# Kernel optimization log

Hardware: AMD Instinct MI355X
Metric: run time of the kernel (lower is better)

The kernel has to match this reference:

```python
import jax, jax.numpy as jnp
import numpy as np

N_NODES, N_EDGES, N_GRAPHS, D = 32768, 49152, 1024, 64


def setup_inputs() -> dict:
    key = jax.random.key(0)
    ks = jax.random.split(key, 24)
    p = lambda k, shape, s=0.1: jax.random.normal(k, shape, dtype=jnp.float32) * s
    return dict(
        x=jax.random.normal(ks[0], (N_NODES, 14), dtype=jnp.float32),
        edge_index=jax.random.randint(ks[1], (2, N_EDGES), 0, N_NODES),
        edge_attr=jax.random.uniform(ks[2], (N_EDGES, 4), dtype=jnp.float32),
        batch=jnp.sort(jax.random.randint(ks[3], (N_NODES,), 0, N_GRAPHS)),
        lin0_W=p(ks[4], (D, 14)), lin0_b=p(ks[5], (D,)),
        e1_W=p(ks[6], (128, 4)), e1_b=p(ks[7], (128,)),
        e2_W=p(ks[8], (D * D, 128), 0.02), e2_b=p(ks[9], (D * D,), 0.02),
        root_W=p(ks[10], (D, D)), conv_b=p(ks[11], (D,)),
        gru_Wih=p(ks[12], (3 * D, D)), gru_Whh=p(ks[13], (3 * D, D)),
        gru_bih=p(ks[14], (3 * D,)), gru_bhh=p(ks[15], (3 * D,)),
        lstm_Wih=p(ks[16], (4 * D, 2 * D)), lstm_Whh=p(ks[17], (4 * D, D)),
        lstm_bih=p(ks[18], (4 * D,)), lstm_bhh=p(ks[19], (4 * D,)),
        fc1_W=p(ks[20], (128, 2 * D)), fc1_b=p(ks[21], (128,)),
        fc2_W=p(ks[22], (1, 128)), fc2_b=p(ks[23], (1,)),
    )


def reference(x, edge_index, edge_attr, batch,
              lin0_W, lin0_b, e1_W, e1_b, e2_W, e2_b, root_W, conv_b,
              gru_Wih, gru_Whh, gru_bih, gru_bhh,
              lstm_Wih, lstm_Whh, lstm_bih, lstm_bhh,
              fc1_W, fc1_b, fc2_W, fc2_b):
    N, B = x.shape[0], N_GRAPHS
    src, dst = edge_index[0], edge_index[1]

    out = jax.nn.relu(x @ lin0_W.T + lin0_b)            # [N, D]
    h = out                                             # GRU hidden (num_layers=1)

    # Edge-conditioned weights: edge_attr is constant across the 3 iterations,
    # so compute the edge MLP once (identical math to re-running it).
    W = jax.nn.relu(edge_attr @ e1_W.T + e1_b) @ e2_W.T + e2_b
    W = W.reshape(-1, D, D)                             # [E, D, D]
    cnt = jnp.maximum(
        jax.ops.segment_sum(jnp.ones((src.shape[0],), x.dtype), dst, num_segments=N), 1.0)

    for _ in range(3):
        # NNConv (aggr='mean'): gather -> per-edge matmul -> scatter-mean -> root + bias
        msg = jnp.einsum('ei,eio->eo', out[src], W)     # [E, D]
        agg = jax.ops.segment_sum(msg, dst, num_segments=N) / cnt[:, None]
        m = jax.nn.relu(agg + out @ root_W + conv_b)
        # GRU cell (seq_len=1)
        gi = m @ gru_Wih.T + gru_bih
        gh = h @ gru_Whh.T + gru_bhh
        ir, iz, inn = jnp.split(gi, 3, -1)
        hr, hz, hn = jnp.split(gh, 3, -1)
        r = jax.nn.sigmoid(ir + hr)
        z = jax.nn.sigmoid(iz + hz)
        n = jnp.tanh(inn + r * hn)
        h = (1.0 - z) * n + z * h
        out = h

    # Set2Set pooling, 3 processing steps, LSTM(2D -> D)
    q_star = jnp.zeros((B, 2 * D), x.dtype)
    hl = jnp.zeros((B, D), x.dtype)
    cl = jnp.zeros((B, D), x.dtype)
    for _ in range(3):
        g = q_star @ lstm_Wih.T + lstm_bih + hl @ lstm_Whh.T + lstm_bhh
        i_, f_, g_, o_ = jnp.split(g, 4, -1)
        cl = jax.nn.sigmoid(f_) * cl + jax.nn.sigmoid(i_) * jnp.tanh(g_)
        hl = jax.nn.sigmoid(o_) * jnp.tanh(cl)
        q = hl                                          # [B, D]
        e = jnp.sum(out * q[batch], -1)                 # [N]
        mx = jax.ops.segment_max(e, batch, num_segments=B)
        ex = jnp.exp(e - mx[batch])
        den = jax.ops.segment_sum(ex, batch, num_segments=B)
        a = ex / den[batch]                             # segment softmax
        r_read = jax.ops.segment_sum(a[:, None] * out, batch, num_segments=B)
        q_star = jnp.concatenate([q, r_read], -1)       # [B, 2D]

    hid = jax.nn.relu(q_star @ fc1_W.T + fc1_b)
    return hid @ fc2_W.T + fc2_b                        # [B, 1]
```

## Files before the change

kernel.cpp:

```cpp
#include <hip/hip_runtime.h>
#include <math.h>

#define NN_ 32768
#define NE_ 49152
#define NG_ 1024

typedef short bh8 __attribute__((ext_vector_type(8)));
typedef float f32x4 __attribute__((ext_vector_type(4)));

__device__ __forceinline__ unsigned short f2bfu(float f) {
    union { float f; unsigned int i; } x; x.f = f;
    unsigned int u = x.i;
    u += 0x7FFFu + ((u >> 16) & 1u);
    return (unsigned short)(u >> 16);
}
__device__ __forceinline__ float sigm(float x) { return 1.f / (1.f + expf(-x)); }

__global__ void MPNN_78632261256134_kernel() {}

__global__ void k_init(int* deg, float* qstar, float* agg) {
    int i = blockIdx.x * 256 + threadIdx.x;
    if (i < NN_) deg[i] = 0;
    int j = i - NN_;
    if (j >= 0 && j < NG_ * 256) qstar[j] = 0.f;
    int k = i - NN_ - NG_ * 256;
    if (k >= 0 && k < NN_ * 64) agg[k] = 0.f;
}

__global__ void k_lin0(const float* x, const float* W, const float* b, float* node) {
    int g = blockIdx.x * 256 + threadIdx.x;
    int n = g >> 6, d = g & 63;
    const float* xr = x + n * 14;
    const float* wr = W + d * 14;
    float acc = b[d];
    for (int i = 0; i < 14; i++) acc += xr[i] * wr[i];
    node[g] = fmaxf(acc, 0.f);
}

__global__ void k_cnt(const int* dst, int* deg) {
    int e = blockIdx.x * 256 + threadIdx.x;
    if (e < NE_) atomicAdd(&deg[dst[e]], 1);
}

__global__ __launch_bounds__(256) void k_scanA(const int* __restrict__ deg,
                                               int* __restrict__ offs,
                                               int* __restrict__ bsum) {
    __shared__ int wtot[4];
    int tid = threadIdx.x, bid = blockIdx.x;
    int i = bid * 256 + tid;
    int v = deg[i];
    int sc = v;
    for (int o = 1; o < 64; o <<= 1) { int u = __shfl_up(sc, o); if ((tid & 63) >= o) sc += u; }
    if ((tid & 63) == 63) wtot[tid >> 6] = sc;
    __syncthreads();
    int wpre = 0;
    for (int k = 0; k < (tid >> 6); k++) wpre += wtot[k];
    offs[i] = sc + wpre - v;
    if (tid == 255) bsum[bid] = sc + wpre;
}

__global__ __launch_bounds__(256) void k_scanC(const int* __restrict__ bsum,
                                               int* __restrict__ offs,
                                               int* __restrict__ head) {
    __shared__ int boff;
    int tid = threadIdx.x, bid = blockIdx.x;
    if (tid == 0) {
        int s = 0;
        for (int k = 0; k < bid; k++) s += bsum[k];
        boff = s;
    }
    __syncthreads();
    int i = bid * 256 + tid;
    int o = offs[i] + boff;
    offs[i] = o; head[i] = o;
    if (i == NN_ - 1) offs[NN_] = NE_;
}

__global__ void k_scatter(const int* __restrict__ dst, int* __restrict__ head,
                          int* __restrict__ perm) {
    int e = blockIdx.x * 256 + threadIdx.x;
    if (e < NE_) { int p = atomicAdd(&head[dst[e]], 1); perm[p] = e; }
}

__global__ void k_gbnd(const int* __restrict__ batch, int* __restrict__ gb) {
    int n = blockIdx.x * 256 + threadIdx.x;
    if (n >= NN_) return;
    int b = batch[n];
    if (n == 0) { for (int g = 0; g <= b; g++) gb[g] = 0; }
    else {
        int pb = batch[n - 1];
        for (int g = pb + 1; g <= b; g++) gb[g] = n;
    }
    if (n == NN_ - 1) { for (int g = b + 1; g <= NG_; g++) gb[g] = NN_; }
}

__global__ void k_tw(const float* gWih, const float* gWhh, float* WihT, float* WhhT,
                     const float* lWih, const float* lWhh, float* WihT2, float* WhhT2) {
    int t = blockIdx.x * 256 + threadIdx.x;
    if (t < 12288) {
        int gr = t >> 6, i = t & 63; WihT[i * 192 + gr] = gWih[t];
    } else if (t < 24576) {
        int u = t - 12288; int gr = u >> 6, i = u & 63; WhhT[i * 192 + gr] = gWhh[u];
    } else if (t < 57344) {
        int u = t - 24576; int r = u >> 7, c = u & 127; WihT2[c * 256 + r] = lWih[u];
    } else if (t < 73728) {
        int u = t - 57344; int r = u >> 6, c = u & 63; WhhT2[c * 256 + r] = lWhh[u];
    }
}

__global__ void k_bhat3(const float* e2W, unsigned short* Bhat3) {
    int idx = blockIdx.x * 256 + threadIdx.x;
    if (idx >= 64 * 4 * 4 * 64 * 8) return;
    int j = idx & 7, lane = (idx >> 3) & 63, t = (idx >> 9) & 3, w = (idx >> 11) & 3, s = idx >> 13;
    int row = s * 64 + w * 16 + (lane & 15);
    int k = t * 32 + (lane >> 4) * 8 + j;
    Bhat3[idx] = f2bfu(e2W[row * 128 + k]);
}

__global__ __launch_bounds__(256) void k_he(const float* __restrict__ ea,
                                            const float* __restrict__ e1W,
                                            const float* __restrict__ e1b,
                                            const int* __restrict__ perm,
                                            unsigned short* __restrict__ Hhat) {
    int tid = threadIdx.x;
    int lane = tid & 63, sub = tid >> 6;
    int gi = blockIdx.x * 4 + sub;
    int etile = gi >> 2, t = gi & 3;
    int e = etile * 16 + (lane & 15), quad = lane >> 4;
    int eo = perm[e];
    const float* ar = ea + (size_t)eo * 4;
    float a0 = ar[0], a1 = ar[1], a2 = ar[2], a3 = ar[3];
    union { unsigned short u[8]; uint4 q; } o;
#pragma unroll
    for (int j = 0; j < 8; j++) {
        int c = t * 32 + quad * 8 + j;
        const float* wr = e1W + c * 4;
        float h = e1b[c] + a0 * wr[0] + a1 * wr[1] + a2 * wr[2] + a3 * wr[3];
        o.u[j] = f2bfu(fmaxf(h, 0.f));
    }
    *(uint4*)(Hhat + (size_t)gi * 512 + lane * 8) = o.q;
}

#define PS(S) (((S) + soff) & 63)

#define LDB(B, S) {                                                                       \
        const unsigned short* _p = Bhat3 + (size_t)PS(S) * 8192 + w * 2048 + lane * 8;    \
        (B)[0] = *(const bh8*)(const void*)(_p);                                          \
        (B)[1] = *(const bh8*)(const void*)(_p + 512);                                    \
        (B)[2] = *(const bh8*)(const void*)(_p + 1024);                                   \
        (B)[3] = *(const bh8*)(const void*)(_p + 1536); }

#define LDXV(XV, S) {                                                                     \
        int sp_ = PS(S);                                                                  \
        _Pragma("unroll")                                                                 \
        for (int mt_ = 0; mt_ < 4; mt_++)                                                 \
            (XV)[mt_] = *(const f32x4*)(const void*)(xs + sp_ * 68 + mt_ * 16 + quad * 4); }

#define LDBB(BB, S) (BB) = e2b[PS(S) * 64 + w * 16 + mrow];

#define MFMA16(ACC, B) {                                                                  \
        __builtin_amdgcn_s_setprio(1);                                                    \
        _Pragma("unroll")                                                                 \
        for (int t_ = 0; t_ < 4; t_++) {                                                  \
            _Pragma("unroll")                                                             \
            for (int mt_ = 0; mt_ < 4; mt_++)                                             \
                (ACC)[mt_] = __builtin_amdgcn_mfma_f32_16x16x32_bf16(                     \
                    af[mt_][t_], (B)[t_], (t_ == 0) ? z4 : (ACC)[mt_], 0, 0, 0);          \
        }                                                                                 \
        __builtin_amdgcn_s_setprio(0); }

#define CONSUME(ACC, XV, BB) {                                                            \
        _Pragma("unroll")                                                                 \
        for (int mt_ = 0; mt_ < 4; mt_++) {                                               \
            _Pragma("unroll")                                                             \
            for (int r_ = 0; r_ < 4; r_++)                                                \
                msgv[mt_][r_] += (XV)[mt_][r_] * ((ACC)[mt_][r_] + (BB));                 \
        } }

__global__ __launch_bounds__(256, 2) void k_convr(const float* __restrict__ node,
                                                  const unsigned short* __restrict__ Hhat,
                                                  const unsigned short* __restrict__ Bhat3,
                                                  const float* __restrict__ e2b,
                                                  const int* __restrict__ src,
                                                  const int* __restrict__ dst,
                                                  const int* __restrict__ perm,
                                                  float* __restrict__ agg) {
    __shared__ __align__(16) float xs[64 * 68];
    __shared__ int dst_s[64];

    const int tid = threadIdx.x;
    const int eb = blockIdx.x * 64;
    const int lane = tid & 63, w = tid >> 6;
    const int quad = lane >> 4, mrow = lane & 15;
    const int soff = (blockIdx.x * 37) & 63;

    {
        int r = tid >> 2, c = tid & 3;
        int s = src[perm[eb + r]];
        const float* nr = node + (size_t)s * 64 + c * 16;
#pragma unroll
        for (int j = 0; j < 16; j++) xs[(c * 16 + j) * 68 + r] = nr[j];
        if (tid < 64) dst_s[tid] = dst[perm[eb + tid]];
    }

    bh8 af[4][4];
#pragma unroll
    for (int mt = 0; mt < 4; mt++)
#pragma unroll
        for (int t = 0; t < 4; t++)
            af[mt][t] = *(const bh8*)(const void*)(
                Hhat + (size_t)(((eb >> 4) + mt) * 4 + t) * 512 + lane * 8);
    __syncthreads();

    const f32x4 z4 = {0.f, 0.f, 0.f, 0.f};
    f32x4 msgv[4];
#pragma unroll
    for (int mt = 0; mt < 4; mt++) msgv[mt] = z4;

    bh8 b0[4], b1[4];
    f32x4 xvA[4], xvB[4];
    f32x4 accA[4], accB[4];
    float bbA, bbB;

    LDB(b0, 0)
    LDB(b1, 1)
    LDXV(xvA, 0)
    LDBB(bbA, 0)
    MFMA16(accA, b0)
    LDB(b0, 2)

#pragma unroll 1
    for (int s = 0; s < 62; s += 2) {
        MFMA16(accB, b1)
        LDB(b1, s + 3)
        LDXV(xvB, s + 1)
        LDBB(bbB, s + 1)
        CONSUME(accA, xvA, bbA)
        MFMA16(accA, b0)
        LDB(b0, (s + 4) & 63)
        LDXV(xvA, s + 2)
        LDBB(bbA, s + 2)
        CONSUME(accB, xvB, bbB)
    }
    MFMA16(accB, b1)
    CONSUME(accA, xvA, bbA)
    LDXV(xvB, 63)
    LDBB(bbB, 63)
    CONSUME(accB, xvB, bbB)

    __syncthreads();
#pragma unroll
    for (int mt = 0; mt < 4; mt++)
#pragma unroll
        for (int r = 0; r < 4; r++)
            xs[(mt * 16 + quad * 4 + r) * 68 + w * 16 + mrow] = msgv[mt][r];
    __syncthreads();
    {
        const int ebase = w * 16;
        const int d = lane;
        float acc = 0.f;
        int startE = ebase;
        int curn = dst_s[ebase];
#pragma unroll
        for (int e = ebase; e < ebase + 16; e++) {
            acc += xs[e * 68 + d];
            int nxt = (e < ebase + 15) ? dst_s[e + 1] : -1;
            if (nxt != curn) {
                float* dp = agg + (size_t)curn * 64 + d;
                if (startE == ebase || e == ebase + 15) atomicAdd(dp, acc);
                else *dp = acc;
                acc = 0.f; startE = e + 1; curn = nxt;
            }
        }
    }
}

__global__ __launch_bounds__(256) void k_mgru(float* __restrict__ agg,
                                              const int* __restrict__ offs,
                                              const float* __restrict__ node,
                                              const float* __restrict__ rootW,
                                              const float* __restrict__ convb,
                                              const float* __restrict__ WihT,
                                              const float* __restrict__ WhhT,
                                              const float* __restrict__ bih,
                                              const float* __restrict__ bhh,
                                              float* __restrict__ hOut) {
    __shared__ __align__(16) float hsT[64][20];
    __shared__ __align__(16) float msT[64][20];
    const int tid = threadIdx.x;
    const int d = tid & 63, sub = tid >> 6;
    const int nb = blockIdx.x * 16;
    const int r0 = sub * 4;
    const int off = (blockIdx.x * 37) & 63;

    {
        f32x4 hv;
#pragma unroll
        for (int j = 0; j < 4; j++)
            hv[j] = node[(size_t)(nb + r0 + j) * 64 + d];
        *(f32x4*)&hsT[d][r0] = hv;
    }
    __syncthreads();

    {
        f32x4 root = {0.f, 0.f, 0.f, 0.f};
        for (int ii = 0; ii < 64; ii++) {
            int i = (ii + off) & 63;
            float wv = rootW[i * 64 + d];
            f32x4 h4 = *(const f32x4*)&hsT[i][r0];
#pragma unroll
            for (int j = 0; j < 4; j++) root[j] += h4[j] * wv;
        }
        float cb = convb[d];
        f32x4 mval;
#pragma unroll
        for (int j = 0; j < 4; j++) {
            int n = nb + r0 + j;
            float dg = (float)(offs[n + 1] - offs[n]);
            float inv = 1.f / fmaxf(dg, 1.f);
            float av = agg[(size_t)n * 64 + d];
            agg[(size_t)n * 64 + d] = 0.f;
            mval[j] = fmaxf(av * inv + cb + root[j], 0.f);
        }
        *(f32x4*)&msT[d][r0] = mval;
    }
    __syncthreads();

    float ir[4], iz[4], in_[4], hr[4], hz[4], hn[4];
    {
        float bi0 = bih[d], bi1 = bih[64 + d], bi2 = bih[128 + d];
        float bh0 = bhh[d], bh1 = bhh[64 + d], bh2 = bhh[128 + d];
#pragma unroll
        for (int j = 0; j < 4; j++) {
            ir[j] = bi0; iz[j] = bi1; in_[j] = bi2;
            hr[j] = bh0; hz[j] = bh1; hn[j] = bh2;
        }
    }
    for (int ii = 0; ii < 64; ii++) {
        int i = (ii + off) & 63;
        float wi0 = WihT[i * 192 + d];
        float wi1 = WihT[i * 192 + 64 + d];
        float wi2 = WihT[i * 192 + 128 + d];
        float wh0 = WhhT[i * 192 + d];
        float wh1 = WhhT[i * 192 + 64 + d];
        float wh2 = WhhT[i * 192 + 128 + d];
        f32x4 m4 = *(const f32x4*)&msT[i][r0];
        f32x4 h4 = *(const f32x4*)&hsT[i][r0];
#pragma unroll
        for (int j = 0; j < 4; j++) {
            ir[j] += m4[j] * wi0; iz[j] += m4[j] * wi1; in_[j] += m4[j] * wi2;
            hr[j] += h4[j] * wh0; hz[j] += h4[j] * wh1; hn[j] += h4[j] * wh2;
        }
    }
    f32x4 hold = *(const f32x4*)&hsT[d][r0];
#pragma unroll
    for (int j = 0; j < 4; j++) {
        float r = sigm(ir[j] + hr[j]);
        float z = sigm(iz[j] + hz[j]);
        float nn = tanhf(in_[j] + r * hn[j]);
        hOut[(size_t)(nb + r0 + j) * 64 + d] = (1.f - z) * nn + z * hold[j];
    }
}

__global__ __launch_bounds__(256) void k_s2s(const float* __restrict__ node,
                                             const int* __restrict__ gb,
                                             const float* __restrict__ WihT2,
                                             const float* __restrict__ WhhT2,
                                             const float* __restrict__ bih,
                                             const float* __restrict__ bhh,
                                             float* __restrict__ cl,
                                             float* __restrict__ hl,
                                             float* __restrict__ qstar) {
    __shared__ float qvs[128];
    __shared__ float hls[64];
    __shared__ float accs[4][64];
    __shared__ float qsh[64];
    __shared__ float mW[4], lW[4];
    __shared__ float rW[4][64];
    const int b = blockIdx.x, tid = threadIdx.x;
    const int lane = tid & 63, wv = tid >> 6;

    if (tid < 128) qvs[tid] = qstar[(size_t)b * 128 + tid];
    else if (tid < 192) hls[tid - 128] = hl[(size_t)b * 64 + (tid - 128)];
    __syncthreads();

    {
        float acc = bih[wv * 64 + lane] + bhh[wv * 64 + lane];
        const float* wih = WihT2 + wv * 64 + lane;
        const float* whh = WhhT2 + wv * 64 + lane;
#pragma unroll 4
        for (int j = 0; j < 128; j++) acc += qvs[j] * wih[(size_t)j * 256];
#pragma unroll 4
        for (int j = 0; j < 64; j++) acc += hls[j] * whh[(size_t)j * 256];
        accs[wv][lane] = acc;
    }
    __syncthreads();

    if (tid < 64) {
        float c = sigm(accs[1][tid]) * cl[(size_t)b * 64 + tid]
                + sigm(accs[0][tid]) * tanhf(accs[2][tid]);
        cl[(size_t)b * 64 + tid] = c;
        float q = sigm(accs[3][tid]) * tanhf(c);
        hl[(size_t)b * 64 + tid] = q;
        qsh[tid] = q;
    }
    __syncthreads();
    const float q = qsh[lane];

    const int start = gb[b], end = gb[b + 1];

    float r_acc = 0.f, m_run = -1e30f, l_run = 0.f;
    for (int n = start + wv; n < end; n += 4) {
        float nv = node[(size_t)n * 64 + lane];
        float p = nv * q;
#pragma unroll
        for (int o = 32; o > 0; o >>= 1) p += __shfl_xor(p, o);
        float m_new = fmaxf(m_run, p);
        float sc = expf(m_run - m_new);
        float wgt = expf(p - m_new);
        l_run = l_run * sc + wgt;
        r_acc = r_acc * sc + wgt * nv;
        m_run = m_new;
    }
    rW[wv][lane] = r_acc;
    if (lane == 0) { mW[wv] = m_run; lW[wv] = l_run; }
    __syncthreads();

    if (tid < 64) {
        float m = fmaxf(fmaxf(mW[0], mW[1]), fmaxf(mW[2], mW[3]));
        float l = 0.f, r = 0.f;
#pragma unroll
        for (int i = 0; i < 4; i++) {
            float sc = expf(mW[i] - m);
            l += lW[i] * sc;
            r += rW[i][tid] * sc;
        }
        qstar[(size_t)b * 128 + tid] = qsh[tid];
        qstar[(size_t)b * 128 + 64 + tid] = (end > start) ? r / l : 0.f;
    }
}

__global__ void k_fc(const float* qstar, const float* W1, const float* b1,
                     const float* W2, const float* b2, float* out) {
    __shared__ float hid[128];
    int b = blockIdx.x; int t = threadIdx.x;
    const float* qr = qstar + (size_t)b * 128;
    float acc = b1[t];
    const float* wr = W1 + (size_t)t * 128;
    for (int k = 0; k < 128; k++) acc += qr[k] * wr[k];
    hid[t] = fmaxf(acc, 0.f);
    __syncthreads();
    if (t < 64) {
        float s = hid[t] * W2[t] + hid[t + 64] * W2[t + 64];
        for (int o = 32; o > 0; o >>= 1) s += __shfl_xor(s, o);
        if (t == 0) out[b] = s + b2[0];
    }
}

extern "C" void kernel_launch(void* const* d_in, const int* in_sizes, int n_in,
                              void* d_out, int out_size, void* d_ws, size_t ws_size,
                              hipStream_t stream) {
    const float* x     = (const float*)d_in[0];
    const int*   ei    = (const int*)d_in[1];
    const float* ea    = (const float*)d_in[2];
    const int*   batch = (const int*)d_in[3];
    const float* lin0W = (const float*)d_in[4];
    const float* lin0b = (const float*)d_in[5];
    const float* e1W   = (const float*)d_in[6];
    const float* e1b   = (const float*)d_in[7];
    const float* e2W   = (const float*)d_in[8];
    const float* e2b   = (const float*)d_in[9];
    const float* rootW = (const float*)d_in[10];
    const float* convb = (const float*)d_in[11];
    const float* gWih  = (const float*)d_in[12];
    const float* gWhh  = (const float*)d_in[13];
    const float* gbih  = (const float*)d_in[14];
    const float* gbhh  = (const float*)d_in[15];
    const float* lWih  = (const float*)d_in[16];
    const float* lWhh  = (const float*)d_in[17];
    const float* lbih  = (const float*)d_in[18];
    const float* lbhh  = (const float*)d_in[19];
    const float* fc1W  = (const float*)d_in[20];
    const float* fc1b  = (const float*)d_in[21];
    const float* fc2W  = (const float*)d_in[22];
    const float* fc2b  = (const float*)d_in[23];
    const int* src = ei;
    const int* dst = ei + NE_;

    char* p = (char*)d_ws;
    auto alloc = [&](size_t bytes) -> char* {
        char* r = p; p += (bytes + 255) & ~(size_t)255; return r;
    };
    unsigned short* Bhat3 = (unsigned short*)alloc((size_t)524288 * 2);
    unsigned short* Hhat  = (unsigned short*)alloc((size_t)NE_ * 128 * 2);
    float* nodeA  = (float*)alloc((size_t)NN_ * 64 * 4);
    float* nodeB  = (float*)alloc((size_t)NN_ * 64 * 4);
    float* aggb   = (float*)alloc((size_t)NN_ * 64 * 4);
    int*   deg    = (int*)alloc((size_t)NN_ * 4);
    int*   offs   = (int*)alloc((size_t)(NN_ + 1) * 4);
    int*   head   = (int*)alloc((size_t)NN_ * 4);
    int*   perm   = (int*)alloc((size_t)NE_ * 4);
    int*   bsum   = (int*)alloc((size_t)128 * 4);
    int*   gb     = (int*)alloc((size_t)(NG_ + 1) * 4);
    float* WihT   = (float*)alloc(192 * 64 * 4);
    float* WhhT   = (float*)alloc(192 * 64 * 4);
    float* WihT2  = (float*)alloc(256 * 128 * 4);
    float* WhhT2  = (float*)alloc(256 * 64 * 4);
    float* qstar  = (float*)alloc((size_t)NG_ * 128 * 4);
    float* hl     = (float*)alloc((size_t)NG_ * 64 * 4);
    float* clb    = (float*)alloc((size_t)NG_ * 64 * 4);

    k_init<<<(NN_ + NG_ * 256 + NN_ * 64 + 255) / 256, 256, 0, stream>>>(deg, qstar, aggb);
    k_lin0<<<NN_ * 64 / 256, 256, 0, stream>>>(x, lin0W, lin0b, nodeA);
    k_cnt<<<NE_ / 256, 256, 0, stream>>>(dst, deg);
    k_scanA<<<NN_ / 256, 256, 0, stream>>>(deg, offs, bsum);
    k_scanC<<<NN_ / 256, 256, 0, stream>>>(bsum, offs, head);
    k_scatter<<<NE_ / 256, 256, 0, stream>>>(dst, head, perm);
    k_gbnd<<<NN_ / 256, 256, 0, stream>>>(batch, gb);
    k_tw<<<288, 256, 0, stream>>>(gWih, gWhh, WihT, WhhT, lWih, lWhh, WihT2, WhhT2);
    k_bhat3<<<524288 / 256, 256, 0, stream>>>(e2W, Bhat3);
    k_he<<<NE_ / 16, 256, 0, stream>>>(ea, e1W, e1b, perm, Hhat);

    float* curF = nodeA; float* nxtF = nodeB;
    for (int it = 0; it < 3; it++) {
        k_convr<<<NE_ / 64, 256, 0, stream>>>(curF, Hhat, Bhat3, e2b, src, dst, perm, aggb);
        k_mgru<<<NN_ / 16, 256, 0, stream>>>(aggb, offs, curF, rootW, convb,
                                             WihT, WhhT, gbih, gbhh, nxtF);
        float* tf = curF; curF = nxtF; nxtF = tf;
    }

    for (int s = 0; s < 3; s++)
        k_s2s<<<NG_, 256, 0, stream>>>(curF, gb, WihT2, WhhT2, lbih, lbhh, clb, hl, qstar);
    k_fc<<<NG_, 128, 0, stream>>>(qstar, fc1W, fc1b, fc2W, fc2b, (float*)d_out);
}
```

Measured before the change: 472.2 us.

## Process 128 edges per conv block to reuse each streamed B tile twice

The edge-conditioned conv kernel now handles 128 edges per block instead of 64. It holds two sets of A fragments so every Bhat3 tile loaded from global memory feeds two MFMA groups. This halves the B-tile traffic per edge and the number of blocks, and the node rows are now gathered with 16-byte vector loads. The cost is much higher register pressure (af doubles, two accumulator and message sets), a simpler non-prefetching software pipeline that may expose load latency, fewer blocks for occupancy, and a larger shared buffer.

```diff
diff --git a/kernel.cpp b/kernel.cpp
--- a/kernel.cpp
+++ b/kernel.cpp
@@ -150,31 +150,26 @@
         (B)[2] = *(const bh8*)(const void*)(_p + 1024);                                   \
         (B)[3] = *(const bh8*)(const void*)(_p + 1536); }
 
-#define LDXV(XV, S) {                                                                     \
-        int sp_ = PS(S);                                                                  \
-        _Pragma("unroll")                                                                 \
-        for (int mt_ = 0; mt_ < 4; mt_++)                                                 \
-            (XV)[mt_] = *(const f32x4*)(const void*)(xs + sp_ * 68 + mt_ * 16 + quad * 4); }
-
-#define LDBB(BB, S) (BB) = e2b[PS(S) * 64 + w * 16 + mrow];
-
-#define MFMA16(ACC, B) {                                                                  \
+#define MFMA16(ACC, H, B) {                                                               \
         __builtin_amdgcn_s_setprio(1);                                                    \
         _Pragma("unroll")                                                                 \
         for (int t_ = 0; t_ < 4; t_++) {                                                  \
             _Pragma("unroll")                                                             \
             for (int mt_ = 0; mt_ < 4; mt_++)                                             \
                 (ACC)[mt_] = __builtin_amdgcn_mfma_f32_16x16x32_bf16(                     \
-                    af[mt_][t_], (B)[t_], (t_ == 0) ? z4 : (ACC)[mt_], 0, 0, 0);          \
+                    af[H][mt_][t_], (B)[t_], (t_ == 0) ? z4 : (ACC)[mt_], 0, 0, 0);       \
         }                                                                                 \
         __builtin_amdgcn_s_setprio(0); }
 
-#define CONSUME(ACC, XV, BB) {                                                            \
+#define CONSUME(ACC, MSG, H, S, BB) {                                                     \
+        int sp_ = PS(S);                                                                  \
         _Pragma("unroll")                                                                 \
         for (int mt_ = 0; mt_ < 4; mt_++) {                                               \
+            f32x4 xv_ = *(const f32x4*)(const void*)(                                     \
+                xs + sp_ * 136 + (H) * 64 + mt_ * 16 + quad * 4);                         \
             _Pragma("unroll")                                                             \
             for (int r_ = 0; r_ < 4; r_++)                                                \
-                msgv[mt_][r_] += (XV)[mt_][r_] * ((ACC)[mt_][r_] + (BB));                 \
+                (MSG)[mt_][r_] += xv_[r_] * ((ACC)[mt_][r_] + (BB));                      \
         } }
 
 __global__ __launch_bounds__(256, 2) void k_convr(const float* __restrict__ node,
@@ -185,78 +180,77 @@
                                                   const int* __restrict__ dst,
                                                   const int* __restrict__ perm,
                                                   float* __restrict__ agg) {
-    __shared__ __align__(16) float xs[64 * 68];
-    __shared__ int dst_s[64];
+    __shared__ __align__(16) float xs[64 * 136];
+    __shared__ int dst_s[128];
 
     const int tid = threadIdx.x;
-    const int eb = blockIdx.x * 64;
+    const int eb = blockIdx.x * 128;
     const int lane = tid & 63, w = tid >> 6;
     const int quad = lane >> 4, mrow = lane & 15;
     const int soff = (blockIdx.x * 37) & 63;
 
     {
-        int r = tid >> 2, c = tid & 3;
+        int r = tid >> 1, c = tid & 1;
         int s = src[perm[eb + r]];
-        const float* nr = node + (size_t)s * 64 + c * 16;
-#pragma unroll
-        for (int j = 0; j < 16; j++) xs[(c * 16 + j) * 68 + r] = nr[j];
-        if (tid < 64) dst_s[tid] = dst[perm[eb + tid]];
-    }
-
-    bh8 af[4][4];
+        const float* nr = node + (size_t)s * 64 + c * 32;
+#pragma unroll
+        for (int j4 = 0; j4 < 8; j4++) {
+            f32x4 v = *(const f32x4*)(nr + j4 * 4);
+#pragma unroll
+            for (int k = 0; k < 4; k++)
+                xs[(c * 32 + j4 * 4 + k) * 136 + r] = v[k];
+        }
+        if (tid < 128) dst_s[tid] = dst[perm[eb + tid]];
+    }
+
+    bh8 af[2][4][4];
+#pragma unroll
+    for (int h = 0; h < 2; h++)
+#pragma unroll
+        for (int mt = 0; mt < 4; mt++)
+#pragma unroll
+            for (int t = 0; t < 4; t++)
+                af[h][mt][t] = *(const bh8*)(const void*)(
+                    Hhat + (size_t)(((eb >> 4) + h * 4 + mt) * 4 + t) * 512 + lane * 8);
+    __syncthreads();
+
+    const f32x4 z4 = {0.f, 0.f, 0.f, 0.f};
+    f32x4 msg0[4], msg1[4];
+#pragma unroll
+    for (int mt = 0; mt < 4; mt++) { msg0[mt] = z4; msg1[mt] = z4; }
+
+    bh8 b0[4], b1[4];
+    f32x4 acc0[4], acc1[4];
+
+    LDB(b0, 0)
+#pragma unroll 1
+    for (int s = 0; s < 64; s += 2) {
+        if (s + 1 < 64) LDB(b1, s + 1)
+        float bb = e2b[PS(s) * 64 + w * 16 + mrow];
+        MFMA16(acc0, 0, b0)
+        MFMA16(acc1, 1, b0)
+        CONSUME(acc0, msg0, 0, s, bb)
+        CONSUME(acc1, msg1, 1, s, bb)
+        if (s + 2 < 64) LDB(b0, s + 2)
+        float bb2 = e2b[PS(s + 1) * 64 + w * 16 + mrow];
+        MFMA16(acc0, 0, b1)
+        MFMA16(acc1, 1, b1)
+        CONSUME(acc0, msg0, 0, s + 1, bb2)
+        CONSUME(acc1, msg1, 1, s + 1, bb2)
+    }
+
+    __syncthreads();
 #pragma unroll
     for (int mt = 0; mt < 4; mt++)
 #pragma unroll
-        for (int t = 0; t < 4; t++)
-            af[mt][t] = *(const bh8*)(const void*)(
-                Hhat + (size_t)(((eb >> 4) + mt) * 4 + t) * 512 + lane * 8);
-    __syncthreads();
-
-    const f32x4 z4 = {0.f, 0.f, 0.f, 0.f};
-    f32x4 msgv[4];
-#pragma unroll
-    for (int mt = 0; mt < 4; mt++) msgv[mt] = z4;
-
-    bh8 b0[4], b1[4];
-    f32x4 xvA[4], xvB[4];
-    f32x4 accA[4], accB[4];
-    float bbA, bbB;
-
-    LDB(b0, 0)
-    LDB(b1, 1)
-    LDXV(xvA, 0)
-    LDBB(bbA, 0)
-    MFMA16(accA, b0)
-    LDB(b0, 2)
-
-#pragma unroll 1
-    for (int s = 0; s < 62; s += 2) {
-        MFMA16(accB, b1)
-        LDB(b1, s + 3)
-        LDXV(xvB, s + 1)
-        LDBB(bbB, s + 1)
-        CONSUME(accA, xvA, bbA)
-        MFMA16(accA, b0)
-        LDB(b0, (s + 4) & 63)
-        LDXV(xvA, s + 2)
-        LDBB(bbA, s + 2)
-        CONSUME(accB, xvB, bbB)
-    }
-    MFMA16(accB, b1)
-    CONSUME(accA, xvA, bbA)
-    LDXV(xvB, 63)
-    LDBB(bbB, 63)
-    CONSUME(accB, xvB, bbB)
-
-    __syncthreads();
-#pragma unroll
-    for (int mt = 0; mt < 4; mt++)
-#pragma unroll
-        for (int r = 0; r < 4; r++)
-            xs[(mt * 16 + quad * 4 + r) * 68 + w * 16 + mrow] = msgv[mt][r];
-    __syncthreads();
-    {
-        const int ebase = w * 16;
+        for (int r = 0; r < 4; r++) {
+            xs[(mt * 16 + quad * 4 + r) * 68 + w * 16 + mrow] = msg0[mt][r];
+            xs[(64 + mt * 16 + quad * 4 + r) * 68 + w * 16 + mrow] = msg1[mt][r];
+        }
+    __syncthreads();
+#pragma unroll
+    for (int win = 0; win < 2; win++) {
+        const int ebase = (w * 2 + win) * 16;
         const int d = lane;
         float acc = 0.f;
         int startE = ebase;
@@ -523,7 +517,7 @@
 
     float* curF = nodeA; float* nxtF = nodeB;
     for (int it = 0; it < 3; it++) {
-        k_convr<<<NE_ / 64, 256, 0, stream>>>(curF, Hhat, Bhat3, e2b, src, dst, perm, aggb);
+        k_convr<<<NE_ / 128, 256, 0, stream>>>(curF, Hhat, Bhat3, e2b, src, dst, perm, aggb);
         k_mgru<<<NN_ / 16, 256, 0, stream>>>(aggb, offs, curF, rootW, convb,
                                              WihT, WhhT, gbih, gbhh, nxtF);
         float* tf = curF; curF = nxtF; nxtF = tf;
```

New measurement: 532.6 us. 1.13x slower.

## Fuse three Set2Set steps into one kernel with chunked block-wide softmax

Applied to the files above, without the earlier changes.

Merges the three per-step Set2Set launches into one kernel that keeps the LSTM state (h, c, q_star) in shared memory, which removes two launches and the global round-trips for cl/hl/qstar. It skips the LSTM matmul on the first step, where the inputs are zero, and drops the qstar zeroing from the init kernel. The online softmax now works on chunks of up to 256 nodes: scores are stored in shared memory, then the max and sum are reduced across the block. This adds several __syncthreads per chunk and reads each node row twice per step.

```diff
diff --git a/kernel.cpp b/kernel.cpp
--- a/kernel.cpp
+++ b/kernel.cpp
@@ -18,12 +18,10 @@
 
 __global__ void MPNN_78632261256134_kernel() {}
 
-__global__ void k_init(int* deg, float* qstar, float* agg) {
+__global__ void k_init(int* deg, float* agg) {
     int i = blockIdx.x * 256 + threadIdx.x;
     if (i < NN_) deg[i] = 0;
-    int j = i - NN_;
-    if (j >= 0 && j < NG_ * 256) qstar[j] = 0.f;
-    int k = i - NN_ - NG_ * 256;
+    int k = i - NN_;
     if (k >= 0 && k < NN_ * 64) agg[k] = 0.f;
 }
 
@@ -362,82 +360,97 @@
     }
 }
 
-__global__ __launch_bounds__(256) void k_s2s(const float* __restrict__ node,
-                                             const int* __restrict__ gb,
-                                             const float* __restrict__ WihT2,
-                                             const float* __restrict__ WhhT2,
-                                             const float* __restrict__ bih,
-                                             const float* __restrict__ bhh,
-                                             float* __restrict__ cl,
-                                             float* __restrict__ hl,
-                                             float* __restrict__ qstar) {
+__global__ __launch_bounds__(256) void k_s2s3(const float* __restrict__ node,
+                                              const int* __restrict__ gb,
+                                              const float* __restrict__ WihT2,
+                                              const float* __restrict__ WhhT2,
+                                              const float* __restrict__ bih,
+                                              const float* __restrict__ bhh,
+                                              float* __restrict__ qstar) {
     __shared__ float qvs[128];
-    __shared__ float hls[64];
+    __shared__ float hls[64], cls[64], qsh[64];
     __shared__ float accs[4][64];
-    __shared__ float qsh[64];
-    __shared__ float mW[4], lW[4];
-    __shared__ float rW[4][64];
+    __shared__ float es[256];
+    __shared__ float red[4][64];
+    __shared__ float sred[4];
     const int b = blockIdx.x, tid = threadIdx.x;
     const int lane = tid & 63, wv = tid >> 6;
-
-    if (tid < 128) qvs[tid] = qstar[(size_t)b * 128 + tid];
-    else if (tid < 192) hls[tid - 128] = hl[(size_t)b * 64 + (tid - 128)];
-    __syncthreads();
-
-    {
+    const int start = gb[b], end = gb[b + 1];
+
+    if (tid < 128) qvs[tid] = 0.f;
+    else if (tid < 192) hls[tid - 128] = 0.f;
+    else cls[tid - 192] = 0.f;
+    __syncthreads();
+
+    for (int step = 0; step < 3; step++) {
         float acc = bih[wv * 64 + lane] + bhh[wv * 64 + lane];
-        const float* wih = WihT2 + wv * 64 + lane;
-        const float* whh = WhhT2 + wv * 64 + lane;
+        if (step > 0) {
+            const float* wih = WihT2 + wv * 64 + lane;
+            const float* whh = WhhT2 + wv * 64 + lane;
 #pragma unroll 4
-        for (int j = 0; j < 128; j++) acc += qvs[j] * wih[(size_t)j * 256];
+            for (int j = 0; j < 128; j++) acc += qvs[j] * wih[(size_t)j * 256];
 #pragma unroll 4
-        for (int j = 0; j < 64; j++) acc += hls[j] * whh[(size_t)j * 256];
+            for (int j = 0; j < 64; j++) acc += hls[j] * whh[(size_t)j * 256];
+        }
         accs[wv][lane] = acc;
-    }
-    __syncthreads();
-
-    if (tid < 64) {
-        float c = sigm(accs[1][tid]) * cl[(size_t)b * 64 + tid]
-                + sigm(accs[0][tid]) * tanhf(accs[2][tid]);
-        cl[(size_t)b * 64 + tid] = c;
-        float q = sigm(accs[3][tid]) * tanhf(c);
-        hl[(size_t)b * 64 + tid] = q;
-        qsh[tid] = q;
-    }
-    __syncthreads();
-    const float q = qsh[lane];
-
-    const int start = gb[b], end = gb[b + 1];
-
-    float r_acc = 0.f, m_run = -1e30f, l_run = 0.f;
-    for (int n = start + wv; n < end; n += 4) {
-        float nv = node[(size_t)n * 64 + lane];
-        float p = nv * q;
-#pragma unroll
-        for (int o = 32; o > 0; o >>= 1) p += __shfl_xor(p, o);
-        float m_new = fmaxf(m_run, p);
-        float sc = expf(m_run - m_new);
-        float wgt = expf(p - m_new);
-        l_run = l_run * sc + wgt;
-        r_acc = r_acc * sc + wgt * nv;
-        m_run = m_new;
-    }
-    rW[wv][lane] = r_acc;
-    if (lane == 0) { mW[wv] = m_run; lW[wv] = l_run; }
-    __syncthreads();
-
-    if (tid < 64) {
-        float m = fmaxf(fmaxf(mW[0], mW[1]), fmaxf(mW[2], mW[3]));
-        float l = 0.f, r = 0.f;
-#pragma unroll
-        for (int i = 0; i < 4; i++) {
-            float sc = expf(mW[i] - m);
-            l += lW[i] * sc;
-            r += rW[i][tid] * sc;
-        }
-        qstar[(size_t)b * 128 + tid] = qsh[tid];
-        qstar[(size_t)b * 128 + 64 + tid] = (end > start) ? r / l : 0.f;
-    }
+        __syncthreads();
+        if (tid < 64) {
+            float c = sigm(accs[1][tid]) * cls[tid] + sigm(accs[0][tid]) * tanhf(accs[2][tid]);
+            cls[tid] = c;
+            float q = sigm(accs[3][tid]) * tanhf(c);
+            hls[tid] = q; qsh[tid] = q;
+        }
+        __syncthreads();
+        const float q = qsh[lane];
+
+        float m_run = -1e30f, l_run = 0.f, r_part = 0.f;
+        for (int cbase = start; cbase < end; cbase += 256) {
+            int cn = min(256, end - cbase);
+            for (int i = wv; i < cn; i += 4) {
+                float nv = node[(size_t)(cbase + i) * 64 + lane];
+                float p = nv * q;
+#pragma unroll
+                for (int o = 32; o > 0; o >>= 1) p += __shfl_xor(p, o);
+                if (lane == 0) es[i] = p;
+            }
+            __syncthreads();
+            float mloc = -1e30f;
+            for (int i = tid; i < cn; i += 256) mloc = fmaxf(mloc, es[i]);
+#pragma unroll
+            for (int o = 32; o > 0; o >>= 1) mloc = fmaxf(mloc, __shfl_xor(mloc, o));
+            if (lane == 0) sred[wv] = mloc;
+            __syncthreads();
+            float m_chunk = fmaxf(fmaxf(sred[0], sred[1]), fmaxf(sred[2], sred[3]));
+            float m_new = fmaxf(m_run, m_chunk);
+            float sc = expf(m_run - m_new);
+            float lloc = 0.f;
+            for (int i = tid; i < cn; i += 256) {
+                float wgt = expf(es[i] - m_new);
+                es[i] = wgt; lloc += wgt;
+            }
+#pragma unroll
+            for (int o = 32; o > 0; o >>= 1) lloc += __shfl_xor(lloc, o);
+            __syncthreads();
+            if (lane == 0) sred[wv] = lloc;
+            __syncthreads();
+            float l_chunk = sred[0] + sred[1] + sred[2] + sred[3];
+            l_run = l_run * sc + l_chunk;
+            r_part *= sc;
+            for (int i = wv; i < cn; i += 4)
+                r_part += es[i] * node[(size_t)(cbase + i) * 64 + lane];
+            m_run = m_new;
+            __syncthreads();
+        }
+        red[wv][lane] = r_part;
+        __syncthreads();
+        if (tid < 64) {
+            float r = red[0][tid] + red[1][tid] + red[2][tid] + red[3][tid];
+            qvs[tid] = qsh[tid];
+            qvs[64 + tid] = (end > start) ? r / l_run : 0.f;
+        }
+        __syncthreads();
+    }
+    if (tid < 128) qstar[(size_t)b * 128 + tid] = qvs[tid];
 }
 
 __global__ void k_fc(const float* qstar, const float* W1, const float* b1,
@@ -507,10 +520,8 @@
     float* WihT2  = (float*)alloc(256 * 128 * 4);
     float* WhhT2  = (float*)alloc(256 * 64 * 4);
     float* qstar  = (float*)alloc((size_t)NG_ * 128 * 4);
-    float* hl     = (float*)alloc((size_t)NG_ * 64 * 4);
-    float* clb    = (float*)alloc((size_t)NG_ * 64 * 4);
-
-    k_init<<<(NN_ + NG_ * 256 + NN_ * 64 + 255) / 256, 256, 0, stream>>>(deg, qstar, aggb);
+
+    k_init<<<(NN_ + NN_ * 64 + 255) / 256, 256, 0, stream>>>(deg, aggb);
     k_lin0<<<NN_ * 64 / 256, 256, 0, stream>>>(x, lin0W, lin0b, nodeA);
     k_cnt<<<NE_ / 256, 256, 0, stream>>>(dst, deg);
     k_scanA<<<NN_ / 256, 256, 0, stream>>>(deg, offs, bsum);
@@ -529,7 +540,6 @@
         float* tf = curF; curF = nxtF; nxtF = tf;
     }
 
-    for (int s = 0; s < 3; s++)
-        k_s2s<<<NG_, 256, 0, stream>>>(curF, gb, WihT2, WhhT2, lbih, lbhh, clb, hl, qstar);
+    k_s2s3<<<NG_, 256, 0, stream>>>(curF, gb, WihT2, WhhT2, lbih, lbhh, qstar);
     k_fc<<<NG_, 128, 0, stream>>>(qstar, fc1W, fc1b, fc2W, fc2b, (float*)d_out);
 }
```

After: 469.0 us. No clear change (-0.7%).
